# Kernel tuning notes

Hardware: AMD Instinct MI355X
Metric: run time of the kernel (lower is better)

The kernel has to match this reference:

```python
import jax, jax.numpy as jnp
import numpy as np

B, S, H, A, M, V, E = 128, 64, 1000, 1000, 500, 30000, 620


def setup_inputs() -> dict:
    key = jax.random.key(0)
    ks = jax.random.split(key, 20)
    sc = 0.02
    return {
        "x": jax.random.randint(ks[0], (B, 1), 0, V),
        "hidden": jax.random.normal(ks[1], (B, H), jnp.float32),
        "outputs": jax.random.normal(ks[2], (B, S, 2 * H), jnp.float32),
        "emb": jax.random.normal(ks[3], (V, E), jnp.float32) * sc,
        "W_hp": jax.random.normal(ks[4], (A, H), jnp.float32) * sc,
        "b_hp": jnp.zeros((A,), jnp.float32),
        "W_op": jax.random.normal(ks[5], (A, 2 * H), jnp.float32) * sc,
        "b_op": jnp.zeros((A,), jnp.float32),
        "v_e": jax.random.normal(ks[6], (A,), jnp.float32) * sc,
        "W_ih": jax.random.normal(ks[7], (3 * H, 2 * H + E), jnp.float32) * sc,
        "W_hh": jax.random.normal(ks[8], (3 * H, H), jnp.float32) * sc,
        "b_ih": jnp.zeros((3 * H,), jnp.float32),
        "b_hh": jnp.zeros((3 * H,), jnp.float32),
        "W_wv": jax.random.normal(ks[9], (2 * M, 2 * H), jnp.float32) * sc,
        "b_wv": jnp.zeros((2 * M,), jnp.float32),
        "W_lh": jax.random.normal(ks[10], (2 * M, H), jnp.float32) * sc,
        "b_lh": jnp.zeros((2 * M,), jnp.float32),
        "W_le": jax.random.normal(ks[11], (2 * M, E), jnp.float32) * sc,
        "b_le": jnp.zeros((2 * M,), jnp.float32),
        "W_pred": jax.random.normal(ks[12], (V, M), jnp.float32) * sc,
        "b_pred": jnp.zeros((V,), jnp.float32),
    }


def reference(x, hidden, outputs, emb, W_hp, b_hp, W_op, b_op, v_e,
              W_ih, W_hh, b_ih, b_hh, W_wv, b_wv, W_lh, b_lh, W_le, b_le,
              W_pred, b_pred):
    # --- Bahdanau attention (broadcast instead of repeat) ---
    h_proj = hidden @ W_hp.T + b_hp                      # [B,A]
    o_proj = jnp.einsum('bsk,ak->bsa', outputs, W_op) + b_op  # [B,S,A]
    energy = jnp.tanh(h_proj[:, None, :] + o_proj) @ v_e # [B,S]
    attn = jax.nn.softmax(energy, axis=1)                # [B,S]
    ctx = jnp.einsum('bs,bsk->bk', attn, outputs)        # [B,2H] weighted_values

    # --- embedding lookup ---
    emb_x = emb[x[:, 0]]                                 # [B,E]

    # --- single-step GRU (PyTorch gate layout: r, z, n) ---
    gru_in = jnp.concatenate([emb_x, ctx], axis=1)       # [B, E+2H]
    gi = gru_in @ W_ih.T + b_ih                          # [B,3H]
    gh = hidden @ W_hh.T + b_hh                          # [B,3H]
    ir, iz, inn = gi[:, :H], gi[:, H:2*H], gi[:, 2*H:]
    hr, hz, hn = gh[:, :H], gh[:, H:2*H], gh[:, 2*H:]
    r = jax.nn.sigmoid(ir + hr)
    z = jax.nn.sigmoid(iz + hz)
    n = jnp.tanh(inn + r * hn)
    h_new = (1.0 - z) * n + z * hidden                   # [B,H]

    # --- maxout combine of three linears ---
    mo_in = (hidden @ W_lh.T + b_lh) + (emb_x @ W_le.T + b_le) + (ctx @ W_wv.T + b_wv)  # [B,2M]
    mo = mo_in.reshape(-1, M, 2).max(axis=2)             # [B,M]

    prediction = mo @ W_pred.T + b_pred                  # [B,V]
    return prediction, h_new
```

## Files before the change

### kernel.cpp

```cpp
#include <hip/hip_runtime.h>
#include <hip/hip_bf16.h>
#include <math.h>

typedef short bf16x8 __attribute__((ext_vector_type(8)));
typedef float f32x4 __attribute__((ext_vector_type(4)));
typedef unsigned short us8 __attribute__((ext_vector_type(8)));
typedef unsigned short us4 __attribute__((ext_vector_type(4)));

namespace {
constexpr int B_ = 128;
constexpr int S_ = 64;
constexpr int H_ = 1000;
constexpr int A_ = 1000;
constexpr int M_ = 500;
constexpr int V_ = 30000;
constexpr int E_ = 620;

constexpr int KP_OUT  = 2048;
constexpr int KP_HP   = 1024;
constexpr int KP_PRED = 512;
constexpr int LD_CAT  = 3712;
constexpr int NP_A    = 1024;
constexpr int NP_3H   = 3072;
constexpr int OROWS   = 8192;

constexpr int Z_HP = 4, Z_GI = 6, Z_GH = 4, Z_MO = 6, Z_OP = 2;

__device__ __forceinline__ unsigned short f2b(float f) {
  __hip_bfloat16 h = __float2bfloat16(f);
  return *reinterpret_cast<unsigned short*>(&h);
}
__device__ __forceinline__ float b2f(unsigned short u) {
  unsigned v = ((unsigned)u) << 16;
  return __uint_as_float(v);
}
__device__ __forceinline__ float sigmoidf_(float x) {
  return 1.0f / (1.0f + __expf(-x));
}
__device__ __forceinline__ void load_lds16(const void* g, void* l) {
  auto gp = reinterpret_cast<const __attribute__((address_space(1))) char*>(
      reinterpret_cast<uintptr_t>(g));
  unsigned loff = (unsigned)(uintptr_t)l;
  auto lp = reinterpret_cast<__attribute__((address_space(3))) char*>(loff);
  __builtin_amdgcn_global_load_lds(gp, lp, 16, 0, 0);
}
}

struct CJob {
  const float* src; unsigned short* dst;
  int nchunks, cpr, Kel, Rs, ld, coff, Wlim, bstart, nblk;
};

__global__ __launch_bounds__(256) void megacast(CJob j0, CJob j1, CJob j2)
{
  const int bid = blockIdx.x;
  CJob j = j0;
  if (bid >= j1.bstart) j = j1;
  if (bid >= j2.bstart) j = j2;

  const int tpj = j.nblk << 8;
  const int base = ((bid - j.bstart) << 8) + (int)threadIdx.x;

  for (int i = base; i < j.nchunks; i += tpj * 2) {
    const int i2 = i + tpj;
    const bool okB = (i2 < j.nchunks);
    const int rA = i / j.cpr;
    const int cA = (i - rA * j.cpr) << 3;
    const int rB = okB ? (i2 / j.cpr) : 0;
    const int cB = okB ? ((i2 - rB * j.cpr) << 3) : 0;
    const bool fA = (rA < j.Rs) && (cA + 8 <= j.Kel);
    const bool fB = okB && (rB < j.Rs) && (cB + 8 <= j.Kel);

    float4 a0, a1, b0, b1;
    if (fA) {
      const float* s = j.src + (size_t)rA * j.Kel + cA;
      a0 = *(const float4*)s; a1 = *(const float4*)(s + 4);
    }
    if (fB) {
      const float* s = j.src + (size_t)rB * j.Kel + cB;
      b0 = *(const float4*)s; b1 = *(const float4*)(s + 4);
    }

    if (fA) {
      us8 o;
      o[0] = f2b(a0.x); o[1] = f2b(a0.y); o[2] = f2b(a0.z); o[3] = f2b(a0.w);
      o[4] = f2b(a1.x); o[5] = f2b(a1.y); o[6] = f2b(a1.z); o[7] = f2b(a1.w);
      *(us8*)(j.dst + (size_t)rA * j.ld + j.coff + cA) = o;
    } else {
      unsigned short* drow = j.dst + (size_t)rA * j.ld + j.coff;
#pragma unroll
      for (int e = 0; e < 8; ++e) {
        const int c = cA + e;
        if (c < j.Wlim) {
          const float v = (rA < j.Rs && c < j.Kel)
                              ? j.src[(size_t)rA * j.Kel + c] : 0.f;
          drow[c] = f2b(v);
        }
      }
    }
    if (okB) {
      if (fB) {
        us8 o;
        o[0] = f2b(b0.x); o[1] = f2b(b0.y); o[2] = f2b(b0.z); o[3] = f2b(b0.w);
        o[4] = f2b(b1.x); o[5] = f2b(b1.y); o[6] = f2b(b1.z); o[7] = f2b(b1.w);
        *(us8*)(j.dst + (size_t)rB * j.ld + j.coff + cB) = o;
      } else {
        unsigned short* drow = j.dst + (size_t)rB * j.ld + j.coff;
#pragma unroll
        for (int e = 0; e < 8; ++e) {
          const int c = cB + e;
          if (c < j.Wlim) {
            const float v = (rB < j.Rs && c < j.Kel)
                                ? j.src[(size_t)rB * j.Kel + c] : 0.f;
            drow[c] = f2b(v);
          }
        }
      }
    }
  }
}

struct SJob {
  const unsigned short* A; int lda;
  const float* B; int ldb;
  int Nv, Kv;
  float* C; int ldc;
  const float* bias; int Ncol;
  int nK, Z, ntiles, bstart;
};

__global__ __launch_bounds__(256, 4) void gemm_skinny(
    SJob j0, SJob j1, SJob j2, SJob j3)
{
  __shared__ __align__(16) char Bs[2][4096];

  const int bid = blockIdx.x;
  SJob j = j0;
  if (bid >= j1.bstart) j = j1;
  if (bid >= j2.bstart) j = j2;
  if (bid >= j3.bstart) j = j3;
  const int lb = bid - j.bstart;
  const int tile = lb % j.ntiles, z = lb / j.ntiles;
  const int n0 = tile * 32;
  const int ks = (int)((long)j.nK * z / j.Z);
  const int ke = (int)((long)j.nK * (z + 1) / j.Z);

  const int t = threadIdx.x, lane = t & 63, wid = t >> 6;
  const int l15 = lane & 15, l4 = lane >> 4;
  const int mrow = (wid & 1) * 64;
  const int whalf = wid >> 1;

  const int srow = t >> 3;
  const int skq = (t & 7) * 8;
  const int grow = n0 + srow;
  const bool rowok = grow < j.Nv;
  const float* Bp = j.B + (size_t)(rowok ? grow : 0) * j.ldb;
  const unsigned swcol = (unsigned)(skq * 2) ^ (((unsigned)srow & 7u) << 4);

  const unsigned short* Arow = j.A + (size_t)(mrow + l15) * j.lda + l4 * 8;
  const int brow = whalf * 16 + l15;
  const unsigned bb = (unsigned)brow * 128;
  const unsigned bsw = (((unsigned)brow & 7u) << 4);

  float4 sf0, sf1;
  auto stage_load = [&](int kst) {
    const int gk = kst * 64 + skq;
    sf0 = make_float4(0.f, 0.f, 0.f, 0.f);
    sf1 = make_float4(0.f, 0.f, 0.f, 0.f);
    if (rowok) {
      if (gk + 8 <= j.Kv) {
        sf0 = *(const float4*)(Bp + gk);
        sf1 = *(const float4*)(Bp + gk + 4);
      } else {
        float tmp[8];
#pragma unroll
        for (int e = 0; e < 8; ++e)
          tmp[e] = (gk + e < j.Kv) ? Bp[gk + e] : 0.f;
        sf0 = make_float4(tmp[0], tmp[1], tmp[2], tmp[3]);
        sf1 = make_float4(tmp[4], tmp[5], tmp[6], tmp[7]);
      }
    }
  };
  auto stage_write = [&](int buf) {
    us8 o;
    o[0] = f2b(sf0.x); o[1] = f2b(sf0.y); o[2] = f2b(sf0.z); o[3] = f2b(sf0.w);
    o[4] = f2b(sf1.x); o[5] = f2b(sf1.y); o[6] = f2b(sf1.z); o[7] = f2b(sf1.w);
    *(us8*)((char*)Bs[buf] + srow * 128 + swcol) = o;
  };

  f32x4 acc[4] = {};
  stage_load(ks);
  stage_write(0);
  __syncthreads();

  for (int kst = ks; kst < ke; ++kst) {
    const int cur = (kst - ks) & 1;
    const bool more = (kst + 1 < ke);
    if (more) stage_load(kst + 1);
    bf16x8 Af[4][2];
#pragma unroll
    for (int kk = 0; kk < 2; ++kk)
#pragma unroll
      for (int mf = 0; mf < 4; ++mf)
        Af[mf][kk] = *(const bf16x8*)(Arow + (size_t)mf * 16 * j.lda +
                                      kst * 64 + kk * 32);
    bf16x8 Bf[2];
#pragma unroll
    for (int kk = 0; kk < 2; ++kk)
      Bf[kk] = *(const bf16x8*)((char*)Bs[cur] + bb +
                                ((unsigned)(kk * 64 + l4 * 16) ^ bsw));
#pragma unroll
    for (int kk = 0; kk < 2; ++kk)
#pragma unroll
      for (int mf = 0; mf < 4; ++mf)
        acc[mf] = __builtin_amdgcn_mfma_f32_16x16x32_bf16(Af[mf][kk], Bf[kk],
                                                          acc[mf], 0, 0, 0);
    if (more) stage_write(cur ^ 1);
    __syncthreads();
  }

  const int c = n0 + whalf * 16 + l15;
  if (j.bias) {
    if (c < j.Ncol) {
      const float bv = j.bias[c];
#pragma unroll
      for (int mf = 0; mf < 4; ++mf) {
        const int r = mrow + mf * 16 + l4 * 4;
#pragma unroll
        for (int q = 0; q < 4; ++q)
          j.C[(size_t)(r + q) * j.ldc + c] = acc[mf][q] + bv;
      }
    }
  } else {
    float* Cz = j.C + (size_t)z * 128 * j.ldc;
#pragma unroll
    for (int mf = 0; mf < 4; ++mf) {
      const int r = mrow + mf * 16 + l4 * 4;
#pragma unroll
      for (int q = 0; q < 4; ++q)
        Cz[(size_t)(r + q) * j.ldc + c] = acc[mf][q];
    }
  }
}

__global__ __launch_bounds__(256, 4) void gemm128_part(
    const unsigned short* __restrict__ Abf, int ldA,
    const unsigned short* __restrict__ Bbf, int ldB,
    unsigned short* __restrict__ Cout, int ldc, int nK)
{
  __shared__ __align__(16) char As[16384];
  __shared__ __align__(16) char Bs[16384];

  const int t = threadIdx.x;
  const int lane = t & 63, wid = t >> 6;
  const int wm = wid >> 1, wn = wid & 1;
  const int l15 = lane & 15, l4 = lane >> 4;
  const int m0 = blockIdx.x * 128;
  const int n0 = blockIdx.y * 128;
  const int z = blockIdx.z, Z = gridDim.z;
  const int ks = (int)((long)nK * z / Z), ke = (int)((long)nK * (z + 1) / Z);

  f32x4 acc[4][4] = {};

  for (int kst = ks; kst < ke; ++kst) {
    const int k0 = kst * 64;
#pragma unroll
    for (int c = 0; c < 4; ++c) {
      const unsigned ou = c * 4096 + wid * 1024;
      const unsigned oo = ou + lane * 16;
      const unsigned row = oo >> 7, cb = oo & 127u;
      const unsigned scb = cb ^ ((row & 7u) << 4);
      load_lds16((const char*)Abf + ((size_t)(m0 + row) * ldA + k0) * 2 + scb,
                 As + ou);
    }
#pragma unroll
    for (int c = 0; c < 4; ++c) {
      const unsigned ou = c * 4096 + wid * 1024;
      const unsigned oo = ou + lane * 16;
      const unsigned row = oo >> 7, cb = oo & 127u;
      const unsigned scb = cb ^ ((row & 7u) << 4);
      load_lds16((const char*)Bbf + ((size_t)(n0 + row) * ldB + k0) * 2 + scb,
                 Bs + ou);
    }
    __syncthreads();

#pragma unroll
    for (int kk = 0; kk < 2; ++kk) {
      bf16x8 af[4], bfr[4];
#pragma unroll
      for (int i = 0; i < 4; ++i) {
        const unsigned ra = wm * 64 + i * 16 + l15;
        const unsigned ca = (unsigned)(kk * 64 + l4 * 16) ^ ((ra & 7u) << 4);
        af[i] = *(const bf16x8*)(As + ra * 128 + ca);
        const unsigned rb = wn * 64 + i * 16 + l15;
        const unsigned cb2 = (unsigned)(kk * 64 + l4 * 16) ^ ((rb & 7u) << 4);
        bfr[i] = *(const bf16x8*)(Bs + rb * 128 + cb2);
      }
#pragma unroll
      for (int i = 0; i < 4; ++i)
#pragma unroll
        for (int jj = 0; jj < 4; ++jj)
          acc[i][jj] = __builtin_amdgcn_mfma_f32_16x16x32_bf16(af[i], bfr[jj],
                                                               acc[i][jj], 0, 0, 0);
    }
    __syncthreads();
  }

  unsigned short* Cz = Cout + (size_t)z * OROWS * ldc;
#pragma unroll
  for (int i = 0; i < 4; ++i) {
    const int r = m0 + wm * 64 + i * 16 + l4 * 4;
#pragma unroll
    for (int jj = 0; jj < 4; ++jj) {
      const int c = n0 + wn * 64 + jj * 16 + l15;
#pragma unroll
      for (int q = 0; q < 4; ++q)
        Cz[(size_t)(r + q) * ldc + c] = f2b(acc[i][jj][q]);
    }
  }
}

__global__ __launch_bounds__(256) void hp_combine(
    const float* __restrict__ hp, const float* __restrict__ b_op,
    const float* __restrict__ b_hp, float* __restrict__ hpc)
{
  const int idx = blockIdx.x * 256 + threadIdx.x;
  if (idx >= B_ * NP_A) return;
  const int c = idx & (NP_A - 1);
  float s = (c < A_) ? (b_op[c] + b_hp[c]) : 0.f;
#pragma unroll
  for (int zz = 0; zz < Z_HP; ++zz) s += hp[(size_t)zz * B_ * NP_A + idx];
  hpc[idx] = s;
}

__global__ __launch_bounds__(256) void energy_reduce(
    const unsigned short* __restrict__ opart, const float* __restrict__ hpc,
    const float* __restrict__ ve, float* __restrict__ energy)
{
  const int r = blockIdx.x;
  const int b = r >> 6;
  const int t = threadIdx.x;
  float s = 0.f;
  if (t < 250) {
    const int c0 = t * 4;
    const us4 v0 = *(const us4*)(opart + (size_t)r * NP_A + c0);
    const us4 v1 = *(const us4*)(opart + (size_t)OROWS * NP_A + (size_t)r * NP_A + c0);
    const float4 h = *(const float4*)(hpc + (size_t)b * NP_A + c0);
    const float4 vv = *(const float4*)(ve + c0);
    s = tanhf(b2f(v0[0]) + b2f(v1[0]) + h.x) * vv.x
      + tanhf(b2f(v0[1]) + b2f(v1[1]) + h.y) * vv.y
      + tanhf(b2f(v0[2]) + b2f(v1[2]) + h.z) * vv.z
      + tanhf(b2f(v0[3]) + b2f(v1[3]) + h.w) * vv.w;
  }
#pragma unroll
  for (int w = 1; w < 64; w <<= 1) s += __shfl_xor(s, w);
  __shared__ float red[4];
  if ((t & 63) == 0) red[t >> 6] = s;
  __syncthreads();
  if (t == 0) energy[r] = red[0] + red[1] + red[2] + red[3];
}

__global__ __launch_bounds__(256) void softmax_ctx_cat(
    const float* __restrict__ energy, const unsigned short* __restrict__ outb,
    const float* __restrict__ hidden, const float* __restrict__ emb,
    const int* __restrict__ x, unsigned short* __restrict__ cat3)
{
  const int b = blockIdx.x, yq = blockIdx.y;
  const int t = threadIdx.x;
  __shared__ float attn[S_];
  __shared__ float sinv_s;

  if (t < 64) {
    const float e = energy[b * S_ + t];
    float m = e;
#pragma unroll
    for (int w = 1; w < 64; w <<= 1) m = fmaxf(m, __shfl_xor(m, w));
    const float p = __expf(e - m);
    float s = p;
#pragma unroll
    for (int w = 1; w < 64; w <<= 1) s += __shfl_xor(s, w);
    attn[t] = p;
    if (t == 0) sinv_s = 1.f / s;
  }
  __syncthreads();
  const float inv = sinv_s;
  unsigned short* catb = cat3 + (size_t)b * LD_CAT;

  {
    const int c0 = (250 * yq) / 4, c1 = (250 * (yq + 1)) / 4;
    const unsigned short* ob = outb + (size_t)b * S_ * KP_OUT;
    for (int kk = c0 + t; kk < c1; kk += 256) {
      float a[8] = {0.f, 0.f, 0.f, 0.f, 0.f, 0.f, 0.f, 0.f};
      for (int s = 0; s < S_; ++s) {
        const float w = attn[s];
        const us8 v = *(const us8*)(ob + (size_t)s * KP_OUT + kk * 8);
#pragma unroll
        for (int jj = 0; jj < 8; ++jj) a[jj] = fmaf(w, b2f(v[jj]), a[jj]);
      }
      us4 lo, hi;
#pragma unroll
      for (int jj = 0; jj < 4; ++jj) {
        lo[jj] = f2b(a[jj] * inv); hi[jj] = f2b(a[jj + 4] * inv);
      }
      *(us4*)(catb + 1620 + kk * 8) = lo;
      *(us4*)(catb + 1620 + kk * 8 + 4) = hi;
    }
  }
  {
    const int c0 = (250 * yq) / 4, c1 = (250 * (yq + 1)) / 4;
    for (int kk = c0 + t; kk < c1; kk += 256) {
      const float4 f = *(const float4*)(hidden + (size_t)b * H_ + kk * 4);
      us4 v; v[0] = f2b(f.x); v[1] = f2b(f.y); v[2] = f2b(f.z); v[3] = f2b(f.w);
      *(us4*)(catb + kk * 4) = v;
    }
  }
  {
    const int xi = x[b];
    const int c0 = (155 * yq) / 4, c1 = (155 * (yq + 1)) / 4;
    for (int kk = c0 + t; kk < c1; kk += 256) {
      const float4 f = *(const float4*)(emb + (size_t)xi * E_ + kk * 4);
      us4 v; v[0] = f2b(f.x); v[1] = f2b(f.y); v[2] = f2b(f.z); v[3] = f2b(f.w);
      *(us4*)(catb + 1000 + kk * 4) = v;
    }
  }
  if (yq == 3) {
    for (int kk = t; kk < 23; kk += 256) {
      us4 v; v[0] = 0; v[1] = 0; v[2] = 0; v[3] = 0;
      *(us4*)(catb + 3620 + kk * 4) = v;
    }
  }
}

__global__ __launch_bounds__(256) void gru_combine(
    const float* __restrict__ gi, const float* __restrict__ gh,
    const float* __restrict__ b_ih, const float* __restrict__ b_hh,
    const float* __restrict__ hidden, float* __restrict__ hout)
{
  const int idx = blockIdx.x * 256 + threadIdx.x;
  if (idx >= B_ * H_) return;
  const int b = idx / H_, h = idx - b * H_;
  float ir = b_ih[h], iz = b_ih[H_ + h], in = b_ih[2 * H_ + h];
  float hr = b_hh[h], hz = b_hh[H_ + h], hn = b_hh[2 * H_ + h];
#pragma unroll
  for (int zz = 0; zz < Z_GI; ++zz) {
    const float* g = gi + (size_t)zz * B_ * NP_3H + (size_t)b * NP_3H;
    ir += g[h]; iz += g[H_ + h]; in += g[2 * H_ + h];
  }
#pragma unroll
  for (int zz = 0; zz < Z_GH; ++zz) {
    const float* g = gh + (size_t)zz * B_ * NP_3H + (size_t)b * NP_3H;
    hr += g[h]; hz += g[H_ + h]; hn += g[2 * H_ + h];
  }
  const float r = sigmoidf_(ir + hr);
  const float zg = sigmoidf_(iz + hz);
  const float n = tanhf(in + r * hn);
  hout[idx] = (1.f - zg) * n + zg * hidden[idx];
}

__global__ __launch_bounds__(256) void maxpair_cast(
    const float* __restrict__ mo_in,
    const float* __restrict__ b_lh, const float* __restrict__ b_le,
    const float* __restrict__ b_wv, unsigned short* __restrict__ mo_bf)
{
  const int idx = blockIdx.x * 256 + threadIdx.x;
  if (idx >= B_ * KP_PRED) return;
  const int r = idx >> 9, c = idx & 511;
  unsigned short o = 0;
  if (c < M_) {
    const int j0 = 2 * c, j1 = 2 * c + 1;
    float v0 = b_lh[j0] + b_le[j0] + b_wv[j0];
    float v1 = b_lh[j1] + b_le[j1] + b_wv[j1];
#pragma unroll
    for (int zz = 0; zz < Z_MO; ++zz) {
      const float* g = mo_in + (size_t)zz * B_ * NP_A + (size_t)r * NP_A;
      v0 += g[j0]; v1 += g[j1];
    }
    o = f2b(fmaxf(v0, v1));
  }
  mo_bf[idx] = o;
}

extern "C" void kernel_launch(void* const* d_in, const int* in_sizes, int n_in,
                              void* d_out, int out_size, void* d_ws, size_t ws_size,
                              hipStream_t stream)
{
  const int*   x       = (const int*)  d_in[0];
  const float* hidden  = (const float*)d_in[1];
  const float* outputs = (const float*)d_in[2];
  const float* emb     = (const float*)d_in[3];
  const float* W_hp    = (const float*)d_in[4];
  const float* b_hp    = (const float*)d_in[5];
  const float* W_op    = (const float*)d_in[6];
  const float* b_op    = (const float*)d_in[7];
  const float* v_e     = (const float*)d_in[8];
  const float* W_ih    = (const float*)d_in[9];
  const float* W_hh    = (const float*)d_in[10];
  const float* b_ih    = (const float*)d_in[11];
  const float* b_hh    = (const float*)d_in[12];
  const float* W_wv    = (const float*)d_in[13];
  const float* b_wv    = (const float*)d_in[14];
  const float* W_lh    = (const float*)d_in[15];
  const float* b_lh    = (const float*)d_in[16];
  const float* W_le    = (const float*)d_in[17];
  const float* b_le    = (const float*)d_in[18];
  const float* W_pred  = (const float*)d_in[19];
  const float* b_pred  = (const float*)d_in[20];

  char* w = (char*)d_ws;
  auto alloc = [&](size_t bytes) {
    char* p = w; w += (bytes + 255) & ~(size_t)255; return p;
  };
  unsigned short* outputs_bf = (unsigned short*)alloc((size_t)OROWS * KP_OUT * 2);
  unsigned short* W_op_bf    = (unsigned short*)alloc((size_t)NP_A * KP_OUT * 2);
  unsigned short* hidden_bf  = (unsigned short*)alloc((size_t)B_ * KP_HP * 2);
  unsigned short* cat3_bf    = (unsigned short*)alloc((size_t)B_ * LD_CAT * 2);
  unsigned short* mo_bf      = (unsigned short*)alloc((size_t)B_ * KP_PRED * 2);
  float* hp     = (float*)alloc((size_t)Z_HP * B_ * NP_A * 4);
  float* hpc    = (float*)alloc((size_t)B_ * NP_A * 4);
  float* energy = (float*)alloc((size_t)B_ * S_ * 4);
  float* gh     = (float*)alloc((size_t)Z_GH * B_ * NP_3H * 4);
  char* un = w;
  unsigned short* opart = (unsigned short*)un;
  float* gi     = (float*)un;
  float* mo_in  = gi + (size_t)Z_GI * B_ * NP_3H;

  float* pred = (float*)d_out;
  float* hout = pred + (size_t)B_ * V_;

  const dim3 blk(256);
  const int FAR = 0x7fffffff;
  const SJob dummy = { nullptr, 0, nullptr, 0, 0, 0, nullptr, 0,
                       nullptr, 0, 1, 1, 1, FAR };

  {
    CJob jo  = { outputs, outputs_bf, OROWS * 256, 256, 2000, OROWS,
                 KP_OUT, 0, KP_OUT, 0,    2560 };
    CJob jwo = { W_op,    W_op_bf,    NP_A * 256,  256, 2000, A_,
                 KP_OUT, 0, KP_OUT, 2560, 320 };
    CJob jh  = { hidden,  hidden_bf,  B_ * 128,    128, 1000, B_,
                 KP_HP,  0, KP_HP,  2880, 32 };
    megacast<<<dim3(2912), blk, 0, stream>>>(jo, jwo, jh);
  }

  {
    SJob jhp = { hidden_bf, KP_HP, W_hp, H_, A_, H_, hp, NP_A,
                 nullptr, 0, 16, Z_HP, 32, 0 };
    SJob jgh = { hidden_bf, KP_HP, W_hh, H_, 3 * H_, H_, gh, NP_3H,
                 nullptr, 0, 16, Z_GH, 94, 128 };
    gemm_skinny<<<dim3(504), blk, 0, stream>>>(jhp, jgh, dummy, dummy);
  }
  hp_combine<<<dim3(B_ * NP_A / 256), blk, 0, stream>>>(hp, b_op, b_hp, hpc);

  gemm128_part<<<dim3(64, 8, Z_OP), blk, 0, stream>>>(
      outputs_bf, KP_OUT, W_op_bf, KP_OUT, opart, NP_A, KP_OUT / 64);

  energy_reduce<<<dim3(OROWS), blk, 0, stream>>>(opart, hpc, v_e, energy);

  softmax_ctx_cat<<<dim3(B_, 4), blk, 0, stream>>>(
      energy, outputs_bf, hidden, emb, x, cat3_bf);

  {
    SJob jgi = { cat3_bf + 1000, LD_CAT, W_ih, 2620, 3 * H_, 2620, gi, NP_3H,
                 nullptr, 0, 41, Z_GI, 94, 0 };
    SJob jlh = { cat3_bf, LD_CAT, W_lh, H_, A_, H_,
                 mo_in, NP_A, nullptr, 0, 16, 2, 32, 564 };
    SJob jle = { cat3_bf + 1000, LD_CAT, W_le, E_, A_, E_,
                 mo_in + (size_t)2 * B_ * NP_A, NP_A, nullptr, 0, 10, 1, 32, 628 };
    SJob jwv = { cat3_bf + 1620, LD_CAT, W_wv, 2 * H_, A_, 2 * H_,
                 mo_in + (size_t)3 * B_ * NP_A, NP_A, nullptr, 0, 32, 3, 32, 660 };
    gemm_skinny<<<dim3(756), blk, 0, stream>>>(jgi, jlh, jle, jwv);
  }

  gru_combine<<<dim3((B_ * H_ + 255) / 256), blk, 0, stream>>>(
      gi, gh, b_ih, b_hh, hidden, hout);

  maxpair_cast<<<dim3((B_ * KP_PRED + 255) / 256), blk, 0, stream>>>(
      mo_in, b_lh, b_le, b_wv, mo_bf);

  {
    SJob jpr = { mo_bf, KP_PRED, W_pred, M_, V_, M_, pred, V_,
                 b_pred, V_, 8, 1, 938, 0 };
    gemm_skinny<<<dim3(938), blk, 0, stream>>>(jpr, dummy, dummy, dummy);
  }
}
```

Baseline: 179.6 us.

## Widen skinny GEMM K-stage to 256 with single-buffered LDS staging

The skinny GEMM kernel now stages a 256-wide K block of the fp32 weight operand per iteration instead of a 64-wide one. Each thread issues eight float4 global loads up front, converts them to bf16 into a single 16KB swizzled LDS buffer, then runs eight MFMA sub-steps. The aim is to put more weight loads in flight and cut the number of barriers and loop iterations. In exchange, the double-buffered overlap between the next stage's loads and the current MFMAs is dropped, register pressure rises, and the concatenated activation row stride is padded to 3840 so reads rounded up to 256 stay inside zeroed padding.

```diff
diff --git a/kernel.cpp b/kernel.cpp
--- a/kernel.cpp
+++ b/kernel.cpp
@@ -19,7 +19,7 @@
 constexpr int KP_OUT  = 2048;
 constexpr int KP_HP   = 1024;
 constexpr int KP_PRED = 512;
-constexpr int LD_CAT  = 3712;
+constexpr int LD_CAT  = 3840;
 constexpr int NP_A    = 1024;
 constexpr int NP_3H   = 3072;
 constexpr int OROWS   = 8192;
@@ -126,13 +126,13 @@
   int Nv, Kv;
   float* C; int ldc;
   const float* bias; int Ncol;
-  int nK, Z, ntiles, bstart;
+  int nKB, Z, ntiles, bstart;
 };
 
 __global__ __launch_bounds__(256, 4) void gemm_skinny(
     SJob j0, SJob j1, SJob j2, SJob j3)
 {
-  __shared__ __align__(16) char Bs[2][4096];
+  __shared__ __align__(16) char Bs[16384];
 
   const int bid = blockIdx.x;
   SJob j = j0;
@@ -142,8 +142,8 @@
   const int lb = bid - j.bstart;
   const int tile = lb % j.ntiles, z = lb / j.ntiles;
   const int n0 = tile * 32;
-  const int ks = (int)((long)j.nK * z / j.Z);
-  const int ke = (int)((long)j.nK * (z + 1) / j.Z);
+  const int ks = (int)((long)j.nKB * z / j.Z);
+  const int ke = (int)((long)j.nKB * (z + 1) / j.Z);
 
   const int t = threadIdx.x, lane = t & 63, wid = t >> 6;
   const int l15 = lane & 15, l4 = lane >> 4;
@@ -155,68 +155,63 @@
   const int grow = n0 + srow;
   const bool rowok = grow < j.Nv;
   const float* Bp = j.B + (size_t)(rowok ? grow : 0) * j.ldb;
-  const unsigned swcol = (unsigned)(skq * 2) ^ (((unsigned)srow & 7u) << 4);
+  const unsigned swrow = ((unsigned)srow & 7u) << 4;
 
   const unsigned short* Arow = j.A + (size_t)(mrow + l15) * j.lda + l4 * 8;
   const int brow = whalf * 16 + l15;
-  const unsigned bb = (unsigned)brow * 128;
-  const unsigned bsw = (((unsigned)brow & 7u) << 4);
-
-  float4 sf0, sf1;
-  auto stage_load = [&](int kst) {
-    const int gk = kst * 64 + skq;
-    sf0 = make_float4(0.f, 0.f, 0.f, 0.f);
-    sf1 = make_float4(0.f, 0.f, 0.f, 0.f);
-    if (rowok) {
-      if (gk + 8 <= j.Kv) {
-        sf0 = *(const float4*)(Bp + gk);
-        sf1 = *(const float4*)(Bp + gk + 4);
-      } else {
-        float tmp[8];
-#pragma unroll
-        for (int e = 0; e < 8; ++e)
-          tmp[e] = (gk + e < j.Kv) ? Bp[gk + e] : 0.f;
-        sf0 = make_float4(tmp[0], tmp[1], tmp[2], tmp[3]);
-        sf1 = make_float4(tmp[4], tmp[5], tmp[6], tmp[7]);
-      }
-    }
-  };
-  auto stage_write = [&](int buf) {
-    us8 o;
-    o[0] = f2b(sf0.x); o[1] = f2b(sf0.y); o[2] = f2b(sf0.z); o[3] = f2b(sf0.w);
-    o[4] = f2b(sf1.x); o[5] = f2b(sf1.y); o[6] = f2b(sf1.z); o[7] = f2b(sf1.w);
-    *(us8*)((char*)Bs[buf] + srow * 128 + swcol) = o;
-  };
+  const unsigned bsw = ((unsigned)brow & 7u) << 4;
 
   f32x4 acc[4] = {};
-  stage_load(ks);
-  stage_write(0);
-  __syncthreads();
-
-  for (int kst = ks; kst < ke; ++kst) {
-    const int cur = (kst - ks) & 1;
-    const bool more = (kst + 1 < ke);
-    if (more) stage_load(kst + 1);
-    bf16x8 Af[4][2];
-#pragma unroll
-    for (int kk = 0; kk < 2; ++kk)
+
+  for (int kb = ks; kb < ke; ++kb) {
+    const int k0 = kb * 256;
+    float4 sf[8];
+#pragma unroll
+    for (int s4 = 0; s4 < 4; ++s4) {
+      const int gk = k0 + s4 * 64 + skq;
+      float4 f0 = make_float4(0.f, 0.f, 0.f, 0.f);
+      float4 f1 = make_float4(0.f, 0.f, 0.f, 0.f);
+      if (rowok) {
+        if (gk + 8 <= j.Kv) {
+          f0 = *(const float4*)(Bp + gk);
+          f1 = *(const float4*)(Bp + gk + 4);
+        } else {
+          float tmp[8];
+#pragma unroll
+          for (int e = 0; e < 8; ++e)
+            tmp[e] = (gk + e < j.Kv) ? Bp[gk + e] : 0.f;
+          f0 = make_float4(tmp[0], tmp[1], tmp[2], tmp[3]);
+          f1 = make_float4(tmp[4], tmp[5], tmp[6], tmp[7]);
+        }
+      }
+      sf[2 * s4] = f0; sf[2 * s4 + 1] = f1;
+    }
+    __syncthreads();
+#pragma unroll
+    for (int s4 = 0; s4 < 4; ++s4) {
+      us8 o;
+      o[0] = f2b(sf[2*s4].x);   o[1] = f2b(sf[2*s4].y);
+      o[2] = f2b(sf[2*s4].z);   o[3] = f2b(sf[2*s4].w);
+      o[4] = f2b(sf[2*s4+1].x); o[5] = f2b(sf[2*s4+1].y);
+      o[6] = f2b(sf[2*s4+1].z); o[7] = f2b(sf[2*s4+1].w);
+      const unsigned cb = (unsigned)((s4 * 64 + skq) * 2) ^ swrow;
+      *(us8*)(Bs + srow * 512 + cb) = o;
+    }
+    __syncthreads();
+#pragma unroll
+    for (int ks32 = 0; ks32 < 8; ++ks32) {
+      const bf16x8 Bf = *(const bf16x8*)(Bs + brow * 512 +
+                          (((unsigned)(ks32 * 64 + l4 * 16)) ^ bsw));
+      bf16x8 Af[4];
 #pragma unroll
       for (int mf = 0; mf < 4; ++mf)
-        Af[mf][kk] = *(const bf16x8*)(Arow + (size_t)mf * 16 * j.lda +
-                                      kst * 64 + kk * 32);
-    bf16x8 Bf[2];
-#pragma unroll
-    for (int kk = 0; kk < 2; ++kk)
-      Bf[kk] = *(const bf16x8*)((char*)Bs[cur] + bb +
-                                ((unsigned)(kk * 64 + l4 * 16) ^ bsw));
-#pragma unroll
-    for (int kk = 0; kk < 2; ++kk)
+        Af[mf] = *(const bf16x8*)(Arow + (size_t)mf * 16 * j.lda +
+                                  k0 + ks32 * 32);
 #pragma unroll
       for (int mf = 0; mf < 4; ++mf)
-        acc[mf] = __builtin_amdgcn_mfma_f32_16x16x32_bf16(Af[mf][kk], Bf[kk],
+        acc[mf] = __builtin_amdgcn_mfma_f32_16x16x32_bf16(Af[mf], Bf,
                                                           acc[mf], 0, 0, 0);
-    if (more) stage_write(cur ^ 1);
-    __syncthreads();
+    }
   }
 
   const int c = n0 + whalf * 16 + l15;
@@ -424,7 +419,7 @@
     }
   }
   if (yq == 3) {
-    for (int kk = t; kk < 23; kk += 256) {
+    for (int kk = t; kk < 55; kk += 256) {
       us4 v; v[0] = 0; v[1] = 0; v[2] = 0; v[3] = 0;
       *(us4*)(catb + 3620 + kk * 4) = v;
     }
@@ -544,9 +539,9 @@
 
   {
     SJob jhp = { hidden_bf, KP_HP, W_hp, H_, A_, H_, hp, NP_A,
-                 nullptr, 0, 16, Z_HP, 32, 0 };
+                 nullptr, 0, 4, Z_HP, 32, 0 };
     SJob jgh = { hidden_bf, KP_HP, W_hh, H_, 3 * H_, H_, gh, NP_3H,
-                 nullptr, 0, 16, Z_GH, 94, 128 };
+                 nullptr, 0, 4, Z_GH, 94, 128 };
     gemm_skinny<<<dim3(504), blk, 0, stream>>>(jhp, jgh, dummy, dummy);
   }
   hp_combine<<<dim3(B_ * NP_A / 256), blk, 0, stream>>>(hp, b_op, b_hp, hpc);
@@ -561,13 +556,13 @@
 
   {
     SJob jgi = { cat3_bf + 1000, LD_CAT, W_ih, 2620, 3 * H_, 2620, gi, NP_3H,
-                 nullptr, 0, 41, Z_GI, 94, 0 };
+                 nullptr, 0, 11, Z_GI, 94, 0 };
     SJob jlh = { cat3_bf, LD_CAT, W_lh, H_, A_, H_,
-                 mo_in, NP_A, nullptr, 0, 16, 2, 32, 564 };
+                 mo_in, NP_A, nullptr, 0, 4, 2, 32, 564 };
     SJob jle = { cat3_bf + 1000, LD_CAT, W_le, E_, A_, E_,
-                 mo_in + (size_t)2 * B_ * NP_A, NP_A, nullptr, 0, 10, 1, 32, 628 };
+                 mo_in + (size_t)2 * B_ * NP_A, NP_A, nullptr, 0, 3, 1, 32, 628 };
     SJob jwv = { cat3_bf + 1620, LD_CAT, W_wv, 2 * H_, A_, 2 * H_,
-                 mo_in + (size_t)3 * B_ * NP_A, NP_A, nullptr, 0, 32, 3, 32, 660 };
+                 mo_in + (size_t)3 * B_ * NP_A, NP_A, nullptr, 0, 8, 3, 32, 660 };
     gemm_skinny<<<dim3(756), blk, 0, stream>>>(jgi, jlh, jle, jwv);
   }
 
@@ -579,7 +574,7 @@
 
   {
     SJob jpr = { mo_bf, KP_PRED, W_pred, M_, V_, M_, pred, V_,
-                 b_pred, V_, 8, 1, 938, 0 };
+                 b_pred, V_, 2, 1, 938, 0 };
     gemm_skinny<<<dim3(938), blk, 0, stream>>>(jpr, dummy, dummy, dummy);
   }
 }
```

Result: slower. 183.8 us (+2.3%).

## Replace prediction skinny GEMM with dedicated register-resident-A double-buffered kernel

Applied to the files above, without the earlier changes.

Adds a specialized pred_gemm kernel for the final [128x500]x[500x30000] projection. Each block keeps its share of the bf16 maxout activations in registers for the full K range and streams 64 W_pred rows as fp32 through two swizzled LDS buffers with async loads, converting to bf16 on the fly. It replaces the generic gemm_skinny launch of 938 blocks with 469 blocks. The aim is to cut per-tile A reloads and better overlap the W_pred stream with MFMA, at the cost of high register pressure and lower occupancy.

```diff
diff --git a/kernel.cpp b/kernel.cpp
--- a/kernel.cpp
+++ b/kernel.cpp
@@ -239,6 +239,108 @@
 #pragma unroll
       for (int q = 0; q < 4; ++q)
         Cz[(size_t)(r + q) * j.ldc + c] = acc[mf][q];
+    }
+  }
+}
+
+__global__ __launch_bounds__(256, 2) void pred_gemm(
+    const unsigned short* __restrict__ mo_bf,
+    const float* __restrict__ Wp,
+    const float* __restrict__ bias,
+    float* __restrict__ C)
+{
+  __shared__ __align__(16) char Bs0[32768];
+  __shared__ __align__(16) char Bs1[32768];
+
+  const int t = threadIdx.x, lane = t & 63, wid = t >> 6;
+  const int l15 = lane & 15, l4 = lane >> 4;
+  const int n0 = blockIdx.x * 64;
+  const int mrow = wid * 32;
+
+  bf16x8 af[2][16];
+#pragma unroll
+  for (int ksl = 0; ksl < 16; ++ksl)
+#pragma unroll
+    for (int mf = 0; mf < 2; ++mf)
+      af[mf][ksl] = *(const bf16x8*)(mo_bf +
+          (size_t)(mrow + mf * 16 + l15) * KP_PRED + ksl * 32 + l4 * 8);
+
+  auto stage = [&](int st, char* buf) {
+#pragma unroll
+    for (int i = 0; i < 8; ++i) {
+      const unsigned off = (unsigned)i * 4096 + (unsigned)t * 16;
+      const unsigned row = off >> 11, colb = off & 2047u;
+      const unsigned sc = colb ^ ((row & 7u) << 4);
+      const int rg = n0 + st * 16 + (int)row;
+      const bool ok = (rg < V_) && (sc + 16 <= 2000u);
+      const char* src = ok ? ((const char*)Wp + (size_t)rg * 2000 + sc)
+                           : (const char*)Wp;
+      load_lds16(src, buf + off);
+    }
+  };
+
+  f32x4 acc[4][2] = {};
+
+  stage(0, Bs0);
+  stage(1, Bs1);
+
+#define PWAIT(N) do {                                              \
+    asm volatile("s_waitcnt vmcnt(" #N ")" ::: "memory");          \
+    __builtin_amdgcn_sched_barrier(0);                             \
+    __builtin_amdgcn_s_barrier();                                  \
+  } while (0)
+
+#define PCOMPUTE(T, BUF) do {                                              \
+    const char* Brow_ = (const char*)(BUF) + (unsigned)l15 * 2048;         \
+    const unsigned sw_ = ((unsigned)l15 & 7u) << 4;                        \
+    _Pragma("unroll")                                                      \
+    for (int ksl = 0; ksl < 16; ++ksl) {                                   \
+      const unsigned base_ = (unsigned)(ksl * 128 + l4 * 32);              \
+      const float4 f0_ = *(const float4*)(Brow_ + (base_ ^ sw_));          \
+      const float4 f1_ = *(const float4*)(Brow_ + ((base_ + 16) ^ sw_));   \
+      bf16x8 bf_;                                                          \
+      bf_[0] = (short)f2b(f0_.x); bf_[1] = (short)f2b(f0_.y);              \
+      bf_[2] = (short)f2b(f0_.z); bf_[3] = (short)f2b(f0_.w);              \
+      bf_[4] = (short)f2b(f1_.x); bf_[5] = (short)f2b(f1_.y);              \
+      bf_[6] = (short)f2b(f1_.z); bf_[7] = (short)f2b(f1_.w);              \
+      acc[T][0] = __builtin_amdgcn_mfma_f32_16x16x32_bf16(af[0][ksl], bf_, \
+                                                          acc[T][0], 0, 0, 0); \
+      acc[T][1] = __builtin_amdgcn_mfma_f32_16x16x32_bf16(af[1][ksl], bf_, \
+                                                          acc[T][1], 0, 0, 0); \
+    }                                                                      \
+  } while (0)
+
+  PWAIT(8);
+  PCOMPUTE(0, Bs0);
+  __builtin_amdgcn_s_barrier();
+  stage(2, Bs0);
+
+  PWAIT(8);
+  PCOMPUTE(1, Bs1);
+  __builtin_amdgcn_s_barrier();
+  stage(3, Bs1);
+
+  PWAIT(8);
+  PCOMPUTE(2, Bs0);
+
+  PWAIT(0);
+  PCOMPUTE(3, Bs1);
+
+#undef PWAIT
+#undef PCOMPUTE
+
+#pragma unroll
+  for (int st = 0; st < 4; ++st) {
+    const int c = n0 + st * 16 + l15;
+    if (c < V_) {
+      const float bv = bias[c];
+#pragma unroll
+      for (int mf = 0; mf < 2; ++mf) {
+        const int r = mrow + mf * 16 + l4 * 4;
+#pragma unroll
+        for (int q = 0; q < 4; ++q)
+          C[(size_t)(r + q) * V_ + c] = acc[st][mf][q] + bv;
+      }
     }
   }
 }
@@ -577,9 +679,5 @@
   maxpair_cast<<<dim3((B_ * KP_PRED + 255) / 256), blk, 0, stream>>>(
       mo_in, b_lh, b_le, b_wv, mo_bf);
 
-  {
-    SJob jpr = { mo_bf, KP_PRED, W_pred, M_, V_, M_, pred, V_,
-                 b_pred, V_, 8, 1, 938, 0 };
-    gemm_skinny<<<dim3(938), blk, 0, stream>>>(jpr, dummy, dummy, dummy);
-  }
-}
+  pred_gemm<<<dim3(469), blk, 0, stream>>>(mo_bf, W_pred, b_pred, pred);
+}
```

Result: faster. 161.3 us (median of 2 runs) (-10.2%).
